# Kernel tuning notes

Hardware: AMD Instinct MI355X
Metric: run time of the kernel (lower is better)

## Reference

```python
import jax, jax.numpy as jnp
import numpy as np
import math

N, D, H, E, ED = 2048, 256, 8, 65536, 64
HD = D // H  # head_dim = 32


def _layernorm(x, g, b, eps=1e-5):
    mu = jnp.mean(x, axis=-1, keepdims=True)
    var = jnp.mean((x - mu) ** 2, axis=-1, keepdims=True)
    return (x - mu) * jax.lax.rsqrt(var + eps) * g + b


def setup_inputs() -> dict:
    key = jax.random.key(0)
    ks = jax.random.split(key, 24)
    s = 0.02
    inp = {
        "x": jax.random.normal(ks[0], (N, D), jnp.float32),
        "edge_index": jax.random.randint(ks[1], (2, E), 0, N, jnp.int64),
        "edge_attr": jax.random.normal(ks[2], (E, ED), jnp.float32),
        # attention projections (stored [in, out]; y = x @ W + b)
        "Wq": jax.random.normal(ks[3], (D, D), jnp.float32) * s,
        "bq": jnp.zeros((D,), jnp.float32),
        "Wk": jax.random.normal(ks[4], (D, D), jnp.float32) * s,
        "bk": jnp.zeros((D,), jnp.float32),
        "Wv": jax.random.normal(ks[5], (D, D), jnp.float32) * s,
        "bv": jnp.zeros((D,), jnp.float32),
        "Wo": jax.random.normal(ks[6], (D, D), jnp.float32) * s,
        "bo": jnp.zeros((D,), jnp.float32),
        # edge bias projection: edge_dim -> num_heads
        "We": jax.random.normal(ks[7], (ED, H), jnp.float32) * s,
        "be": jnp.zeros((H,), jnp.float32),
        # FFN
        "W1": jax.random.normal(ks[8], (D, 4 * D), jnp.float32) * s,
        "b1": jnp.zeros((4 * D,), jnp.float32),
        "W2": jax.random.normal(ks[9], (4 * D, D), jnp.float32) * s,
        "b2": jnp.zeros((D,), jnp.float32),
        # layernorms
        "ln1_g": jnp.ones((D,), jnp.float32),
        "ln1_b": jnp.zeros((D,), jnp.float32),
        "ln2_g": jnp.ones((D,), jnp.float32),
        "ln2_b": jnp.zeros((D,), jnp.float32),
    }
    return inp


def reference(x, edge_index, edge_attr, Wq, bq, Wk, bk, Wv, bv, Wo, bo,
              We, be, W1, b1, W2, b2, ln1_g, ln1_b, ln2_g, ln2_b):
    n = x.shape[0]
    scale = math.sqrt(HD)
    src, dst = edge_index[0], edge_index[1]

    residual = x
    h = _layernorm(x, ln1_g, ln1_b)
    Q = (h @ Wq + bq).reshape(n, H, HD)
    K = (h @ Wk + bk).reshape(n, H, HD)
    V = (h @ Wv + bv).reshape(n, H, HD)

    # dense [N, N, H] scores, matching the original einsum
    scores = jnp.einsum('nhd,mhd->nmh', Q, K) / scale

    # adjacency mask with self-loops (scatter .set semantics, like torch assignment)
    diag = jnp.arange(n)
    adj = jnp.zeros((n, n), jnp.bool_).at[src, dst].set(True)
    adj = adj.at[diag, diag].set(True)

    # edge bias scattered into [N, N, H] (assignment semantics)
    edge_bias = edge_attr @ We + be  # [E, H]
    bias = jnp.zeros((n, n, H), scores.dtype).at[src, dst].set(edge_bias)
    scores = scores + bias

    scores = jnp.where(adj[:, :, None], scores, -jnp.inf)
    # softmax over dim=1 (source/key nodes m)
    attn = jax.nn.softmax(scores, axis=1)

    out = jnp.einsum('nmh,mhd->nhd', attn, V).reshape(n, D)
    out = out @ Wo + bo
    x = residual + out

    residual = x
    h2 = _layernorm(x, ln2_g, ln2_b)
    ffn = jax.nn.gelu(h2 @ W1 + b1, approximate=False) @ W2 + b2
    return residual + ffn
```

## Files before the change

kernel.cpp:

```cpp
#include <hip/hip_runtime.h>
#include <math.h>

#define D 256
#define NH 8
#define HD 32
#define EDIM 64

typedef __attribute__((ext_vector_type(8))) short bfrag;
typedef __attribute__((ext_vector_type(4))) float ffrag;

__device__ __forceinline__ unsigned short f2bf(float x) {
  unsigned int u = __float_as_uint(x);
  return (unsigned short)((u + 0x7FFFu + ((u >> 16) & 1u)) >> 16);
}

__global__ __launch_bounds__(256) void prep_kernel(
    const float* __restrict__ s0, const float* __restrict__ s1,
    const float* __restrict__ s2, const float* __restrict__ s3,
    const float* __restrict__ s4, const float* __restrict__ s5,
    unsigned short* __restrict__ d0, unsigned short* __restrict__ d1,
    unsigned short* __restrict__ d2, unsigned short* __restrict__ d3,
    unsigned short* __restrict__ d4, unsigned short* __restrict__ d5,
    const float* __restrict__ x, const float* __restrict__ g,
    const float* __restrict__ b, unsigned short* __restrict__ hbf,
    const int* __restrict__ ei, int* __restrict__ cnt,
    const float* __restrict__ ea, const float* __restrict__ We,
    const float* __restrict__ be, float* __restrict__ eb,
    int N, int E, int CB, int EB) {
  int blk = blockIdx.x;
  int tid = threadIdx.x;
  if (blk < CB) {
    int i = (blk * 256 + tid) * 4;
    const float* s; unsigned short* d; int off;
    if      (i < 65536)  { s = s0; d = d0; off = i; }
    else if (i < 131072) { s = s1; d = d1; off = i - 65536; }
    else if (i < 196608) { s = s2; d = d2; off = i - 131072; }
    else if (i < 262144) { s = s3; d = d3; off = i - 196608; }
    else if (i < 524288) { s = s4; d = d4; off = i - 262144; }
    else if (i < 786432) { s = s5; d = d5; off = i - 524288; }
    else return;
    float4 v = *(const float4*)(s + off);
    *(ushort4*)(d + off) = make_ushort4(f2bf(v.x), f2bf(v.y), f2bf(v.z), f2bf(v.w));
  } else if (blk < CB + N) {
    int row = blk - CB;
    float v = x[row * D + tid];
    float s = v, sq = v * v;
    #pragma unroll
    for (int m = 1; m < 64; m <<= 1) { s += __shfl_xor(s, m); sq += __shfl_xor(sq, m); }
    __shared__ float ps[4], pq[4];
    int wid = tid >> 6, lane = tid & 63;
    if (lane == 0) { ps[wid] = s; pq[wid] = sq; }
    __syncthreads();
    float ts = ps[0] + ps[1] + ps[2] + ps[3];
    float tq = pq[0] + pq[1] + pq[2] + pq[3];
    float mu  = ts * (1.f / D);
    float var = tq * (1.f / D) - mu * mu;
    float inv = 1.f / sqrtf(var + 1e-5f);
    hbf[row * D + tid] = f2bf((v - mu) * inv * g[tid] + b[tid]);
  } else if (blk < CB + N + EB) {
    int e = (blk - CB - N) * 256 + tid;
    if (e < E) atomicAdd(&cnt[ei[e]], 1);
  } else {
    int e = (blk - CB - N - EB) * 256 + tid;
    if (e >= E) return;
    const float* row = ea + (size_t)e * EDIM;
    float acc[NH];
    #pragma unroll
    for (int h = 0; h < NH; h++) acc[h] = be[h];
    #pragma unroll 4
    for (int k = 0; k < EDIM; k++) {
      float r = row[k];
      #pragma unroll
      for (int h = 0; h < NH; h++) acc[h] = fmaf(r, We[k * NH + h], acc[h]);
    }
    #pragma unroll
    for (int h = 0; h < NH; h++) eb[e * NH + h] = acc[h];
  }
}

__global__ __launch_bounds__(256) void scan_kernel(const int* __restrict__ cnt,
    int* __restrict__ rowptr, int* __restrict__ cursor, int N) {
  __shared__ int part[256];
  int tid = threadIdx.x;
  int chunk = (N + 255) / 256;
  int base = tid * chunk;
  int s = 0;
  for (int i = 0; i < chunk; i++) { int idx = base + i; if (idx < N) s += cnt[idx]; }
  part[tid] = s;
  __syncthreads();
  for (int off = 1; off < 256; off <<= 1) {
    int v = (tid >= off) ? part[tid - off] : 0;
    __syncthreads();
    part[tid] += v;
    __syncthreads();
  }
  int run = (tid == 0) ? 0 : part[tid - 1];
  for (int i = 0; i < chunk; i++) {
    int idx = base + i;
    if (idx < N) { rowptr[idx] = run; cursor[idx] = run; run += cnt[idx]; }
  }
  if (tid == 255) rowptr[N] = part[255];
}

__global__ void scatter_kernel(const int* __restrict__ ei, int* __restrict__ cursor,
    int* __restrict__ col, int* __restrict__ eidx, int E) {
  int e = blockIdx.x * 256 + threadIdx.x;
  if (e >= E) return;
  int s = ei[e], d = ei[E + e];
  int p = atomicAdd(&cursor[s], 1);
  col[p] = d; eidx[p] = e;
}

__device__ __forceinline__ void mg_core(const unsigned short* __restrict__ A,
    const unsigned short* __restrict__ B, int K, int Nn, int bm, int bn,
    int kb0, int kb1, unsigned short (*As)[40], unsigned short (*Bt)[40],
    ffrag acc[4]) {
  int tid = threadIdx.x;
  int wid = tid >> 6, lane = tid & 63;
  int lr = lane & 15, lk = lane >> 4;
  int ar = tid >> 2, ak = (tid & 3) * 8;
  int bnn = tid & 63, bkg = tid >> 6;
  for (int kb = kb0; kb < kb1; kb += 32) {
    uint4 av = *(const uint4*)(A + (size_t)(bm + ar) * K + kb + ak);
    *(uint4*)&As[ar][ak] = av;
    unsigned int u[4];
    #pragma unroll
    for (int jj = 0; jj < 4; jj++) {
      unsigned short lo = B[(size_t)(kb + bkg * 8 + 2 * jj)     * Nn + bn + bnn];
      unsigned short hi = B[(size_t)(kb + bkg * 8 + 2 * jj + 1) * Nn + bn + bnn];
      u[jj] = (unsigned int)lo | ((unsigned int)hi << 16);
    }
    *(uint4*)&Bt[bnn][bkg * 8] = make_uint4(u[0], u[1], u[2], u[3]);
    __syncthreads();
    bfrag af = *(const bfrag*)&As[wid * 16 + lr][lk * 8];
    #pragma unroll
    for (int nf = 0; nf < 4; nf++) {
      bfrag bf = *(const bfrag*)&Bt[nf * 16 + lr][lk * 8];
      acc[nf] = __builtin_amdgcn_mfma_f32_16x16x32_bf16(af, bf, acc[nf], 0, 0, 0);
    }
    __syncthreads();
  }
}

__global__ __launch_bounds__(256) void mgemm_qkv(const unsigned short* __restrict__ A,
    const unsigned short* __restrict__ B0, const unsigned short* __restrict__ B1,
    const unsigned short* __restrict__ B2,
    const float* __restrict__ b0, const float* __restrict__ b1, const float* __restrict__ b2,
    float* __restrict__ C0, float* __restrict__ C1, float* __restrict__ C2,
    int M, int Nn, int K) {
  __shared__ __align__(16) unsigned short As[64][40];
  __shared__ __align__(16) unsigned short Bt[64][40];
  int z = blockIdx.z;
  const unsigned short* B = (z == 0) ? B0 : (z == 1) ? B1 : B2;
  const float* bias = (z == 0) ? b0 : (z == 1) ? b1 : b2;
  float* C = (z == 0) ? C0 : (z == 1) ? C1 : C2;
  int bm = blockIdx.y * 64, bn = blockIdx.x * 64;
  ffrag acc[4] = {};
  mg_core(A, B, K, Nn, bm, bn, 0, K, As, Bt, acc);
  int lane = threadIdx.x & 63, wid = threadIdx.x >> 6;
  int lr = lane & 15, lk = lane >> 4;
  #pragma unroll
  for (int nf = 0; nf < 4; nf++) {
    int col = bn + nf * 16 + lr;
    float bv = bias[col];
    #pragma unroll
    for (int i = 0; i < 4; i++) {
      int row = bm + wid * 16 + lk * 4 + i;
      C[(size_t)row * Nn + col] = acc[nf][i] + bv;
    }
  }
}

__global__ __launch_bounds__(256) void mgemm_gelu(const unsigned short* __restrict__ A,
    const unsigned short* __restrict__ B, const float* __restrict__ bias,
    unsigned short* __restrict__ C, int M, int Nn, int K) {
  __shared__ __align__(16) unsigned short As[64][40];
  __shared__ __align__(16) unsigned short Bt[64][40];
  int bm = blockIdx.y * 64, bn = blockIdx.x * 64;
  ffrag acc[4] = {};
  mg_core(A, B, K, Nn, bm, bn, 0, K, As, Bt, acc);
  int lane = threadIdx.x & 63, wid = threadIdx.x >> 6;
  int lr = lane & 15, lk = lane >> 4;
  #pragma unroll
  for (int nf = 0; nf < 4; nf++) {
    int col = bn + nf * 16 + lr;
    float bv = bias[col];
    #pragma unroll
    for (int i = 0; i < 4; i++) {
      int row = bm + wid * 16 + lk * 4 + i;
      float v = acc[nf][i] + bv;
      v = 0.5f * v * (1.f + erff(v * 0.70710678118654752f));
      C[(size_t)row * Nn + col] = f2bf(v);
    }
  }
}

__global__ __launch_bounds__(256) void mgemm_splitk(const unsigned short* __restrict__ A,
    const unsigned short* __restrict__ B, float* __restrict__ P,
    int M, int Nn, int K, int Kslice) {
  __shared__ __align__(16) unsigned short As[64][40];
  __shared__ __align__(16) unsigned short Bt[64][40];
  int z = blockIdx.z;
  int bm = blockIdx.y * 64, bn = blockIdx.x * 64;
  ffrag acc[4] = {};
  mg_core(A, B, K, Nn, bm, bn, z * Kslice, (z + 1) * Kslice, As, Bt, acc);
  float* Pz = P + (size_t)z * M * Nn;
  int lane = threadIdx.x & 63, wid = threadIdx.x >> 6;
  int lr = lane & 15, lk = lane >> 4;
  #pragma unroll
  for (int nf = 0; nf < 4; nf++) {
    int col = bn + nf * 16 + lr;
    #pragma unroll
    for (int i = 0; i < 4; i++) {
      int row = bm + wid * 16 + lk * 4 + i;
      Pz[(size_t)row * Nn + col] = acc[nf][i];
    }
  }
}

__global__ __launch_bounds__(256) void reduce_kernel(const float* __restrict__ P,
    const float* __restrict__ bias, const float* __restrict__ R,
    float* __restrict__ out, int MN, int Nn, int S) {
  int i = blockIdx.x * 256 + threadIdx.x;
  if (i * 4 >= MN) return;
  size_t b = (size_t)i * 4;
  float4 acc = *(const float4*)(P + b);
  for (int s = 1; s < S; s++) {
    float4 p = *(const float4*)(P + (size_t)s * MN + b);
    acc.x += p.x; acc.y += p.y; acc.z += p.z; acc.w += p.w;
  }
  float4 bi = *(const float4*)(bias + (b % Nn));
  float4 r  = *(const float4*)(R + b);
  acc.x += bi.x + r.x; acc.y += bi.y + r.y; acc.z += bi.z + r.z; acc.w += bi.w + r.w;
  *(float4*)(out + b) = acc;
}

__global__ __launch_bounds__(256) void ln2_fused_kernel(const float* __restrict__ P,
    const float* __restrict__ bo, const float* __restrict__ x,
    const float* __restrict__ g, const float* __restrict__ b,
    float* __restrict__ x_mid, unsigned short* __restrict__ hbf, int MN) {
  int row = blockIdx.x;
  int tid = threadIdx.x;
  size_t idx = (size_t)row * D + tid;
  float v = P[idx] + P[(size_t)MN + idx] + bo[tid] + x[idx];
  x_mid[idx] = v;
  float s = v, sq = v * v;
  #pragma unroll
  for (int m = 1; m < 64; m <<= 1) { s += __shfl_xor(s, m); sq += __shfl_xor(sq, m); }
  __shared__ float ps[4], pq[4];
  int wid = tid >> 6, lane = tid & 63;
  if (lane == 0) { ps[wid] = s; pq[wid] = sq; }
  __syncthreads();
  float ts = ps[0] + ps[1] + ps[2] + ps[3];
  float tq = pq[0] + pq[1] + pq[2] + pq[3];
  float mu  = ts * (1.f / D);
  float var = tq * (1.f / D) - mu * mu;
  float inv = 1.f / sqrtf(var + 1e-5f);
  hbf[idx] = f2bf((v - mu) * inv * g[tid] + b[tid]);
}

__global__ __launch_bounds__(256) void attn_kernel(const float* __restrict__ Q,
    const float* __restrict__ Km, const float* __restrict__ Vm,
    const float* __restrict__ eb, const int* __restrict__ rowptr,
    const int* __restrict__ col, const int* __restrict__ eidx,
    unsigned short* __restrict__ out, int N) {
  int wid = threadIdx.x >> 6, lane = threadIdx.x & 63;
  int n = blockIdx.x * 4 + wid;
  if (n >= N) return;
  int h = lane >> 3, j = lane & 7;
  int off = h * HD + j * 4;
  float4 q = *(const float4*)(Q + (size_t)n * D + off);
  int beg = rowptr[n], end = rowptr[n + 1];
  int L = end - beg;
  if (L > 256) L = 256;
  int dv0 = -1, dv1 = -1, dv2 = -1, dv3 = -1;
  int ev0 = -1, ev1 = -1, ev2 = -1, ev3 = -1;
  if (lane       < L) { dv0 = col[beg + lane      ]; ev0 = eidx[beg + lane      ]; }
  if (lane +  64 < L) { dv1 = col[beg + lane +  64]; ev1 = eidx[beg + lane +  64]; }
  if (lane + 128 < L) { dv2 = col[beg + lane + 128]; ev2 = eidx[beg + lane + 128]; }
  if (lane + 192 < L) { dv3 = col[beg + lane + 192]; ev3 = eidx[beg + lane + 192]; }
  bool self_present = __any(dv0 == n) || __any(dv1 == n) ||
                      __any(dv2 == n) || __any(dv3 == n);
  float mrun = -INFINITY, srun = 0.f;
  float4 acc = make_float4(0.f, 0.f, 0.f, 0.f);

#define PROC_EDGE(m_, bias_) {                                                 \
    float4 k4 = *(const float4*)(Km + (size_t)(m_) * D + off);                 \
    float dot = q.x * k4.x + q.y * k4.y + q.z * k4.z + q.w * k4.w;             \
    dot += __shfl_xor(dot, 1); dot += __shfl_xor(dot, 2); dot += __shfl_xor(dot, 4); \
    float sc = fmaf(dot, 0.17677669529663687f, bias_);                         \
    float mnew = fmaxf(mrun, sc);                                              \
    float corr = __expf(mrun - mnew);                                          \
    float pp = __expf(sc - mnew);                                              \
    float4 v4 = *(const float4*)(Vm + (size_t)(m_) * D + off);                 \
    srun = srun * corr + pp;                                                   \
    acc.x = fmaf(acc.x, corr, pp * v4.x);                                      \
    acc.y = fmaf(acc.y, corr, pp * v4.y);                                      \
    acc.z = fmaf(acc.z, corr, pp * v4.z);                                      \
    acc.w = fmaf(acc.w, corr, pp * v4.w);                                      \
    mrun = mnew; }

#define PROC_CHUNK(dvC, evC, base_) {                                          \
    int cl = L - (base_); if (cl > 64) cl = 64;                                \
    for (int ii = 0; ii < cl; ii++) {                                          \
      int d_i = __shfl(dvC, ii);                                               \
      int e_i = __shfl(evC, ii);                                               \
      bool dom = (dv0 == d_i && ev0 > e_i) || (dv1 == d_i && ev1 > e_i) ||     \
                 (dv2 == d_i && ev2 > e_i) || (dv3 == d_i && ev3 > e_i);       \
      if (__any(dom)) continue;                                                \
      float bias_ = eb[(size_t)e_i * NH + h];                                  \
      PROC_EDGE(d_i, bias_);                                                   \
    } }

  PROC_CHUNK(dv0, ev0, 0)
  if (L > 64)  PROC_CHUNK(dv1, ev1, 64)
  if (L > 128) PROC_CHUNK(dv2, ev2, 128)
  if (L > 192) PROC_CHUNK(dv3, ev3, 192)
  if (!self_present) PROC_EDGE(n, 0.f)
#undef PROC_CHUNK
#undef PROC_EDGE

  float inv = 1.f / srun;
  ushort4 o = make_ushort4(f2bf(acc.x * inv), f2bf(acc.y * inv),
                           f2bf(acc.z * inv), f2bf(acc.w * inv));
  *(ushort4*)(out + (size_t)n * D + off) = o;
}

extern "C" void kernel_launch(void* const* d_in, const int* in_sizes, int n_in,
                              void* d_out, int out_size, void* d_ws, size_t ws_size,
                              hipStream_t stream) {
  const float* x    = (const float*)d_in[0];
  const int*   ei   = (const int*)d_in[1];
  const float* ea   = (const float*)d_in[2];
  const float* Wq   = (const float*)d_in[3];  const float* bq = (const float*)d_in[4];
  const float* Wk   = (const float*)d_in[5];  const float* bk = (const float*)d_in[6];
  const float* Wv   = (const float*)d_in[7];  const float* bv = (const float*)d_in[8];
  const float* Wo   = (const float*)d_in[9];  const float* bo = (const float*)d_in[10];
  const float* We   = (const float*)d_in[11]; const float* be = (const float*)d_in[12];
  const float* W1   = (const float*)d_in[13]; const float* b1 = (const float*)d_in[14];
  const float* W2   = (const float*)d_in[15]; const float* b2 = (const float*)d_in[16];
  const float* ln1g = (const float*)d_in[17]; const float* ln1b = (const float*)d_in[18];
  const float* ln2g = (const float*)d_in[19]; const float* ln2b = (const float*)d_in[20];

  int N = in_sizes[0] / D;
  int E = in_sizes[1] / 2;

  char* p = (char*)d_ws;
  auto alloc = [&](size_t bytes) -> char* {
    char* r = p; p += (bytes + 255) & ~(size_t)255; return r;
  };
  unsigned short* hbf    = (unsigned short*)alloc((size_t)N * D * 2);
  float*          Qd     = (float*)         alloc((size_t)N * D * 4);
  float*          Kd     = (float*)         alloc((size_t)N * D * 4);
  float*          Vd     = (float*)         alloc((size_t)N * D * 4);
  unsigned short* attnbf = (unsigned short*)alloc((size_t)N * D * 2);
  float*          x_mid  = (float*)         alloc((size_t)N * D * 4);
  float*          ebuf   = (float*)         alloc((size_t)E * NH * 4);
  unsigned short* tbf    = (unsigned short*)alloc((size_t)N * 4 * D * 2);
  float*          P      = (float*)         alloc((size_t)4 * N * D * 4);
  unsigned short* Wqb    = (unsigned short*)alloc((size_t)D * D * 2);
  unsigned short* Wkb    = (unsigned short*)alloc((size_t)D * D * 2);
  unsigned short* Wvb    = (unsigned short*)alloc((size_t)D * D * 2);
  unsigned short* Wob    = (unsigned short*)alloc((size_t)D * D * 2);
  unsigned short* W1b    = (unsigned short*)alloc((size_t)D * 4 * D * 2);
  unsigned short* W2b    = (unsigned short*)alloc((size_t)4 * D * D * 2);
  int*            cnt    = (int*)           alloc((size_t)N * 4);
  int*            rowptr = (int*)           alloc((size_t)(N + 1) * 4);
  int*            cursor = (int*)           alloc((size_t)N * 4);
  int*            colA   = (int*)           alloc((size_t)E * 4);
  int*            eidxA  = (int*)           alloc((size_t)E * 4);

  hipMemsetAsync(cnt, 0, (size_t)N * 4, stream);

  int MN = N * D;
  int CB = 768;
  int EB = (E + 255) / 256;

  prep_kernel<<<CB + N + 2 * EB, 256, 0, stream>>>(
      Wq, Wk, Wv, Wo, W1, W2, Wqb, Wkb, Wvb, Wob, W1b, W2b,
      x, ln1g, ln1b, hbf, ei, cnt, ea, We, be, ebuf, N, E, CB, EB);
  scan_kernel<<<1, 256, 0, stream>>>(cnt, rowptr, cursor, N);
  scatter_kernel<<<EB, 256, 0, stream>>>(ei, cursor, colA, eidxA, E);
  dim3 g_qkv(D / 64, N / 64, 3);
  mgemm_qkv<<<g_qkv, 256, 0, stream>>>(hbf, Wqb, Wkb, Wvb, bq, bk, bv,
                                       Qd, Kd, Vd, N, D, D);
  attn_kernel<<<(N + 3) / 4, 256, 0, stream>>>(Qd, Kd, Vd, ebuf, rowptr, colA, eidxA,
                                               attnbf, N);
  {
    dim3 g(D / 64, N / 64, 2);
    mgemm_splitk<<<g, 256, 0, stream>>>(attnbf, Wob, P, N, D, D, D / 2);
    ln2_fused_kernel<<<N, 256, 0, stream>>>(P, bo, x, ln2g, ln2b, x_mid, hbf, MN);
  }
  dim3 g_1(4 * D / 64, N / 64, 1);
  mgemm_gelu<<<g_1, 256, 0, stream>>>(hbf, W1b, b1, tbf, N, 4 * D, D);
  {
    dim3 g(D / 64, N / 64, 4);
    mgemm_splitk<<<g, 256, 0, stream>>>(tbf, W2b, P, N, D, 4 * D, D);
    reduce_kernel<<<(MN / 4 + 255) / 256, 256, 0, stream>>>(P, b2, x_mid, (float*)d_out,
                                                            MN, D, 4);
  }
}
```

Measured before the change: 202.3 us.

## Replace CSR build with fixed-slot adjacency and drop split-K GEMMs

Replaces the count/scan/scatter CSR construction with fixed per-node slots of MAXDEG entries, filled by atomic cursor inside the prep kernel. This removes two kernel launches, including a single-block scan. The output-projection and FFN2 GEMMs are no longer split-K and instead fuse bias and residual in the epilogue, which removes the partial buffer and the reduce kernel. The trade-offs are that edges beyond 192 per node are silently dropped, and the non-split GEMMs launch only 128 blocks, with a long K loop for FFN2.

```diff
diff --git a/kernel.cpp b/kernel.cpp
--- a/kernel.cpp
+++ b/kernel.cpp
@@ -5,6 +5,7 @@
 #define NH 8
 #define HD 32
 #define EDIM 64
+#define MAXDEG 192
 
 typedef __attribute__((ext_vector_type(8))) short bfrag;
 typedef __attribute__((ext_vector_type(4))) float ffrag;
@@ -24,6 +25,7 @@
     const float* __restrict__ x, const float* __restrict__ g,
     const float* __restrict__ b, unsigned short* __restrict__ hbf,
     const int* __restrict__ ei, int* __restrict__ cnt,
+    int* __restrict__ colp, int* __restrict__ eidxp,
     const float* __restrict__ ea, const float* __restrict__ We,
     const float* __restrict__ be, float* __restrict__ eb,
     int N, int E, int CB, int EB) {
@@ -59,9 +61,6 @@
     hbf[row * D + tid] = f2bf((v - mu) * inv * g[tid] + b[tid]);
   } else if (blk < CB + N + EB) {
     int e = (blk - CB - N) * 256 + tid;
-    if (e < E) atomicAdd(&cnt[ei[e]], 1);
-  } else {
-    int e = (blk - CB - N - EB) * 256 + tid;
     if (e >= E) return;
     const float* row = ea + (size_t)e * EDIM;
     float acc[NH];
@@ -75,40 +74,16 @@
     }
     #pragma unroll
     for (int h = 0; h < NH; h++) eb[e * NH + h] = acc[h];
-  }
-}
-
-__global__ __launch_bounds__(256) void scan_kernel(const int* __restrict__ cnt,
-    int* __restrict__ rowptr, int* __restrict__ cursor, int N) {
-  __shared__ int part[256];
-  int tid = threadIdx.x;
-  int chunk = (N + 255) / 256;
-  int base = tid * chunk;
-  int s = 0;
-  for (int i = 0; i < chunk; i++) { int idx = base + i; if (idx < N) s += cnt[idx]; }
-  part[tid] = s;
-  __syncthreads();
-  for (int off = 1; off < 256; off <<= 1) {
-    int v = (tid >= off) ? part[tid - off] : 0;
-    __syncthreads();
-    part[tid] += v;
-    __syncthreads();
-  }
-  int run = (tid == 0) ? 0 : part[tid - 1];
-  for (int i = 0; i < chunk; i++) {
-    int idx = base + i;
-    if (idx < N) { rowptr[idx] = run; cursor[idx] = run; run += cnt[idx]; }
-  }
-  if (tid == 255) rowptr[N] = part[255];
-}
-
-__global__ void scatter_kernel(const int* __restrict__ ei, int* __restrict__ cursor,
-    int* __restrict__ col, int* __restrict__ eidx, int E) {
-  int e = blockIdx.x * 256 + threadIdx.x;
-  if (e >= E) return;
-  int s = ei[e], d = ei[E + e];
-  int p = atomicAdd(&cursor[s], 1);
-  col[p] = d; eidx[p] = e;
+  } else {
+    int e = (blk - CB - N - EB) * 256 + tid;
+    if (e >= E) return;
+    int s = ei[e], d = ei[E + e];
+    int pos = atomicAdd(&cnt[s], 1);
+    if (pos < MAXDEG) {
+      colp [(size_t)s * MAXDEG + pos] = d;
+      eidxp[(size_t)s * MAXDEG + pos] = e;
+    }
+  }
 }
 
 __device__ __forceinline__ void mg_core(const unsigned short* __restrict__ A,
@@ -171,6 +146,28 @@
   }
 }
 
+__global__ __launch_bounds__(256) void mgemm_res(const unsigned short* __restrict__ A,
+    const unsigned short* __restrict__ B, const float* __restrict__ bias,
+    const float* __restrict__ R, float* __restrict__ C, int M, int Nn, int K) {
+  __shared__ __align__(16) unsigned short As[64][40];
+  __shared__ __align__(16) unsigned short Bt[64][40];
+  int bm = blockIdx.y * 64, bn = blockIdx.x * 64;
+  ffrag acc[4] = {};
+  mg_core(A, B, K, Nn, bm, bn, 0, K, As, Bt, acc);
+  int lane = threadIdx.x & 63, wid = threadIdx.x >> 6;
+  int lr = lane & 15, lk = lane >> 4;
+  #pragma unroll
+  for (int nf = 0; nf < 4; nf++) {
+    int col = bn + nf * 16 + lr;
+    float bv = bias[col];
+    #pragma unroll
+    for (int i = 0; i < 4; i++) {
+      int row = bm + wid * 16 + lk * 4 + i;
+      C[(size_t)row * Nn + col] = acc[nf][i] + bv + R[(size_t)row * Nn + col];
+    }
+  }
+}
+
 __global__ __launch_bounds__(256) void mgemm_gelu(const unsigned short* __restrict__ A,
     const unsigned short* __restrict__ B, const float* __restrict__ bias,
     unsigned short* __restrict__ C, int M, int Nn, int K) {
@@ -195,55 +192,12 @@
   }
 }
 
-__global__ __launch_bounds__(256) void mgemm_splitk(const unsigned short* __restrict__ A,
-    const unsigned short* __restrict__ B, float* __restrict__ P,
-    int M, int Nn, int K, int Kslice) {
-  __shared__ __align__(16) unsigned short As[64][40];
-  __shared__ __align__(16) unsigned short Bt[64][40];
-  int z = blockIdx.z;
-  int bm = blockIdx.y * 64, bn = blockIdx.x * 64;
-  ffrag acc[4] = {};
-  mg_core(A, B, K, Nn, bm, bn, z * Kslice, (z + 1) * Kslice, As, Bt, acc);
-  float* Pz = P + (size_t)z * M * Nn;
-  int lane = threadIdx.x & 63, wid = threadIdx.x >> 6;
-  int lr = lane & 15, lk = lane >> 4;
-  #pragma unroll
-  for (int nf = 0; nf < 4; nf++) {
-    int col = bn + nf * 16 + lr;
-    #pragma unroll
-    for (int i = 0; i < 4; i++) {
-      int row = bm + wid * 16 + lk * 4 + i;
-      Pz[(size_t)row * Nn + col] = acc[nf][i];
-    }
-  }
-}
-
-__global__ __launch_bounds__(256) void reduce_kernel(const float* __restrict__ P,
-    const float* __restrict__ bias, const float* __restrict__ R,
-    float* __restrict__ out, int MN, int Nn, int S) {
-  int i = blockIdx.x * 256 + threadIdx.x;
-  if (i * 4 >= MN) return;
-  size_t b = (size_t)i * 4;
-  float4 acc = *(const float4*)(P + b);
-  for (int s = 1; s < S; s++) {
-    float4 p = *(const float4*)(P + (size_t)s * MN + b);
-    acc.x += p.x; acc.y += p.y; acc.z += p.z; acc.w += p.w;
-  }
-  float4 bi = *(const float4*)(bias + (b % Nn));
-  float4 r  = *(const float4*)(R + b);
-  acc.x += bi.x + r.x; acc.y += bi.y + r.y; acc.z += bi.z + r.z; acc.w += bi.w + r.w;
-  *(float4*)(out + b) = acc;
-}
-
-__global__ __launch_bounds__(256) void ln2_fused_kernel(const float* __restrict__ P,
-    const float* __restrict__ bo, const float* __restrict__ x,
+__global__ __launch_bounds__(256) void ln2_kernel(const float* __restrict__ x,
     const float* __restrict__ g, const float* __restrict__ b,
-    float* __restrict__ x_mid, unsigned short* __restrict__ hbf, int MN) {
+    unsigned short* __restrict__ out) {
   int row = blockIdx.x;
   int tid = threadIdx.x;
-  size_t idx = (size_t)row * D + tid;
-  float v = P[idx] + P[(size_t)MN + idx] + bo[tid] + x[idx];
-  x_mid[idx] = v;
+  float v = x[row * D + tid];
   float s = v, sq = v * v;
   #pragma unroll
   for (int m = 1; m < 64; m <<= 1) { s += __shfl_xor(s, m); sq += __shfl_xor(sq, m); }
@@ -256,13 +210,13 @@
   float mu  = ts * (1.f / D);
   float var = tq * (1.f / D) - mu * mu;
   float inv = 1.f / sqrtf(var + 1e-5f);
-  hbf[idx] = f2bf((v - mu) * inv * g[tid] + b[tid]);
+  out[row * D + tid] = f2bf((v - mu) * inv * g[tid] + b[tid]);
 }
 
 __global__ __launch_bounds__(256) void attn_kernel(const float* __restrict__ Q,
     const float* __restrict__ Km, const float* __restrict__ Vm,
-    const float* __restrict__ eb, const int* __restrict__ rowptr,
-    const int* __restrict__ col, const int* __restrict__ eidx,
+    const float* __restrict__ eb, const int* __restrict__ cnt,
+    const int* __restrict__ colp, const int* __restrict__ eidxp,
     unsigned short* __restrict__ out, int N) {
   int wid = threadIdx.x >> 6, lane = threadIdx.x & 63;
   int n = blockIdx.x * 4 + wid;
@@ -270,17 +224,15 @@
   int h = lane >> 3, j = lane & 7;
   int off = h * HD + j * 4;
   float4 q = *(const float4*)(Q + (size_t)n * D + off);
-  int beg = rowptr[n], end = rowptr[n + 1];
-  int L = end - beg;
-  if (L > 256) L = 256;
-  int dv0 = -1, dv1 = -1, dv2 = -1, dv3 = -1;
-  int ev0 = -1, ev1 = -1, ev2 = -1, ev3 = -1;
-  if (lane       < L) { dv0 = col[beg + lane      ]; ev0 = eidx[beg + lane      ]; }
-  if (lane +  64 < L) { dv1 = col[beg + lane +  64]; ev1 = eidx[beg + lane +  64]; }
-  if (lane + 128 < L) { dv2 = col[beg + lane + 128]; ev2 = eidx[beg + lane + 128]; }
-  if (lane + 192 < L) { dv3 = col[beg + lane + 192]; ev3 = eidx[beg + lane + 192]; }
-  bool self_present = __any(dv0 == n) || __any(dv1 == n) ||
-                      __any(dv2 == n) || __any(dv3 == n);
+  int L = cnt[n];
+  if (L > MAXDEG) L = MAXDEG;
+  size_t base = (size_t)n * MAXDEG;
+  int dv0 = -1, dv1 = -1, dv2 = -1;
+  int ev0 = -1, ev1 = -1, ev2 = -1;
+  if (lane       < L) { dv0 = colp[base + lane      ]; ev0 = eidxp[base + lane      ]; }
+  if (lane +  64 < L) { dv1 = colp[base + lane +  64]; ev1 = eidxp[base + lane +  64]; }
+  if (lane + 128 < L) { dv2 = colp[base + lane + 128]; ev2 = eidxp[base + lane + 128]; }
+  bool self_present = __any(dv0 == n) || __any(dv1 == n) || __any(dv2 == n);
   float mrun = -INFINITY, srun = 0.f;
   float4 acc = make_float4(0.f, 0.f, 0.f, 0.f);
 
@@ -306,7 +258,7 @@
       int d_i = __shfl(dvC, ii);                                               \
       int e_i = __shfl(evC, ii);                                               \
       bool dom = (dv0 == d_i && ev0 > e_i) || (dv1 == d_i && ev1 > e_i) ||     \
-                 (dv2 == d_i && ev2 > e_i) || (dv3 == d_i && ev3 > e_i);       \
+                 (dv2 == d_i && ev2 > e_i);                                    \
       if (__any(dom)) continue;                                                \
       float bias_ = eb[(size_t)e_i * NH + h];                                  \
       PROC_EDGE(d_i, bias_);                                                   \
@@ -315,7 +267,6 @@
   PROC_CHUNK(dv0, ev0, 0)
   if (L > 64)  PROC_CHUNK(dv1, ev1, 64)
   if (L > 128) PROC_CHUNK(dv2, ev2, 128)
-  if (L > 192) PROC_CHUNK(dv3, ev3, 192)
   if (!self_present) PROC_EDGE(n, 0.f)
 #undef PROC_CHUNK
 #undef PROC_EDGE
@@ -357,7 +308,6 @@
   float*          x_mid  = (float*)         alloc((size_t)N * D * 4);
   float*          ebuf   = (float*)         alloc((size_t)E * NH * 4);
   unsigned short* tbf    = (unsigned short*)alloc((size_t)N * 4 * D * 2);
-  float*          P      = (float*)         alloc((size_t)4 * N * D * 4);
   unsigned short* Wqb    = (unsigned short*)alloc((size_t)D * D * 2);
   unsigned short* Wkb    = (unsigned short*)alloc((size_t)D * D * 2);
   unsigned short* Wvb    = (unsigned short*)alloc((size_t)D * D * 2);
@@ -365,38 +315,26 @@
   unsigned short* W1b    = (unsigned short*)alloc((size_t)D * 4 * D * 2);
   unsigned short* W2b    = (unsigned short*)alloc((size_t)4 * D * D * 2);
   int*            cnt    = (int*)           alloc((size_t)N * 4);
-  int*            rowptr = (int*)           alloc((size_t)(N + 1) * 4);
-  int*            cursor = (int*)           alloc((size_t)N * 4);
-  int*            colA   = (int*)           alloc((size_t)E * 4);
-  int*            eidxA  = (int*)           alloc((size_t)E * 4);
+  int*            colp   = (int*)           alloc((size_t)N * MAXDEG * 4);
+  int*            eidxp  = (int*)           alloc((size_t)N * MAXDEG * 4);
 
   hipMemsetAsync(cnt, 0, (size_t)N * 4, stream);
 
-  int MN = N * D;
   int CB = 768;
   int EB = (E + 255) / 256;
 
   prep_kernel<<<CB + N + 2 * EB, 256, 0, stream>>>(
       Wq, Wk, Wv, Wo, W1, W2, Wqb, Wkb, Wvb, Wob, W1b, W2b,
-      x, ln1g, ln1b, hbf, ei, cnt, ea, We, be, ebuf, N, E, CB, EB);
-  scan_kernel<<<1, 256, 0, stream>>>(cnt, rowptr, cursor, N);
-  scatter_kernel<<<EB, 256, 0, stream>>>(ei, cursor, colA, eidxA, E);
+      x, ln1g, ln1b, hbf, ei, cnt, colp, eidxp, ea, We, be, ebuf, N, E, CB, EB);
   dim3 g_qkv(D / 64, N / 64, 3);
   mgemm_qkv<<<g_qkv, 256, 0, stream>>>(hbf, Wqb, Wkb, Wvb, bq, bk, bv,
                                        Qd, Kd, Vd, N, D, D);
-  attn_kernel<<<(N + 3) / 4, 256, 0, stream>>>(Qd, Kd, Vd, ebuf, rowptr, colA, eidxA,
+  attn_kernel<<<(N + 3) / 4, 256, 0, stream>>>(Qd, Kd, Vd, ebuf, cnt, colp, eidxp,
                                                attnbf, N);
-  {
-    dim3 g(D / 64, N / 64, 2);
-    mgemm_splitk<<<g, 256, 0, stream>>>(attnbf, Wob, P, N, D, D, D / 2);
-    ln2_fused_kernel<<<N, 256, 0, stream>>>(P, bo, x, ln2g, ln2b, x_mid, hbf, MN);
-  }
-  dim3 g_1(4 * D / 64, N / 64, 1);
+  dim3 g_o(D / 64, N / 64);
+  mgemm_res<<<g_o, 256, 0, stream>>>(attnbf, Wob, bo, x, x_mid, N, D, D);
+  ln2_kernel<<<N, 256, 0, stream>>>(x_mid, ln2g, ln2b, hbf);
+  dim3 g_1(4 * D / 64, N / 64);
   mgemm_gelu<<<g_1, 256, 0, stream>>>(hbf, W1b, b1, tbf, N, 4 * D, D);
-  {
-    dim3 g(D / 64, N / 64, 4);
-    mgemm_splitk<<<g, 256, 0, stream>>>(tbf, W2b, P, N, D, 4 * D, D);
-    reduce_kernel<<<(MN / 4 + 255) / 256, 256, 0, stream>>>(P, b2, x_mid, (float*)d_out,
-                                                            MN, D, 4);
-  }
-}
+  mgemm_res<<<g_o, 256, 0, stream>>>(tbf, W2b, b2, x_mid, (float*)d_out, N, D, 4 * D);
+}
```

Measured after the change: 197.6 us. -2.3%, faster.
